# Kernel tuning notes

Hardware: AMD Instinct MI355X
Metric: run time of the kernel (lower is better)

## Reference

```python
import jax, jax.numpy as jnp
import numpy as np

D_K = 64

def setup_inputs() -> dict:
    key = jax.random.key(0)
    kq, kk, kv = jax.random.split(key, 3)
    shape = (2, 16, 2048, D_K)  # [B, H, S, d_k]
    q = jax.random.normal(kq, shape, dtype=jnp.float32)
    k = jax.random.normal(kk, shape, dtype=jnp.float32)
    v = jax.random.normal(kv, shape, dtype=jnp.float32)
    return {"q": q, "k": k, "v": v}

def reference(q, k, v):
    # score = q @ k^T / sqrt(d_k)  -> [B, H, S, S]
    scale = 1.0 / np.sqrt(D_K).astype(np.float32)
    score = jnp.einsum("bhqd,bhkd->bhqk", q, k) * scale
    attn = jax.nn.softmax(score, axis=-1)
    # dropout is identity in eval mode
    out = jnp.einsum("bhqk,bhkd->bhqd", attn, v)
    return out
```

## Files before the change

### kernel.cpp

```cpp
#include <hip/hip_runtime.h>
#include <hip/hip_bf16.h>
#include <math.h>
#include <stdint.h>


#define S_LEN 2048
#define DK 64
#define QW 32
#define NW 4
#define QBLK (QW * NW)
#define KVBLK 64
#define NT (S_LEN / KVBLK)
#define LOG2E 1.44269504088896340736f
#define THR 8.0f

typedef __attribute__((ext_vector_type(16))) float f32x16;
typedef __attribute__((ext_vector_type(8)))  __bf16 bf16x8;
typedef __attribute__((ext_vector_type(4)))  __bf16 bf16x4;
typedef __attribute__((ext_vector_type(4)))  uint32_t u32x4;

union frag_cast { u32x4 u; bf16x8 h; };

__device__ __forceinline__ uint32_t cvt_pk_bf16(float lo, float hi) {
    uint32_t r;
    asm("v_cvt_pk_bf16_f32 %0, %1, %2" : "=v"(r) : "v"(lo), "v"(hi));
    return r;
}
__device__ __forceinline__ void perm32swap(uint32_t& a, uint32_t& b) {
    asm volatile("v_permlane32_swap_b32 %0, %1" : "+v"(a), "+v"(b));
}

__global__ __launch_bounds__(256, 2)
void attn_fwd_kernel(const float* __restrict__ Qg, const float* __restrict__ Kg,
                     const float* __restrict__ Vg, float* __restrict__ Og)
{
    __shared__ __align__(16) __bf16 Kl[2][64 * 64];
    __shared__ __align__(16) __bf16 Vt[2][64 * 64];

    const int tid = threadIdx.x;
    const int lane = tid & 63;
    const int w   = tid >> 6;
    const int l31 = lane & 31;
    const int hi  = lane >> 5;

    const int qt = blockIdx.x;
    const int bh = blockIdx.y;
    const size_t base = (size_t)bh * (S_LEN * DK);
    const int q0g = qt * QBLK + w * QW;

    bf16x8 qf[4];
    {
        const float sc = 0.125f * LOG2E;
        const float* qrow = Qg + base + (size_t)(q0g + l31) * DK;
        #pragma unroll
        for (int sp = 0; sp < 4; ++sp) {
            const int d0 = 16 * sp + 8 * hi;
            float4 a = *(const float4*)(qrow + d0);
            float4 b = *(const float4*)(qrow + d0 + 4);
            bf16x8 f;
            f[0] = (__bf16)(a.x * sc); f[1] = (__bf16)(a.y * sc);
            f[2] = (__bf16)(a.z * sc); f[3] = (__bf16)(a.w * sc);
            f[4] = (__bf16)(b.x * sc); f[5] = (__bf16)(b.y * sc);
            f[6] = (__bf16)(b.z * sc); f[7] = (__bf16)(b.w * sc);
            qf[sp] = f;
        }
    }

    f32x16 acc0 = {}, acc1 = {};
    float m_run = -INFINITY, l_run = 0.f;

    float4 kpre[4];
    float  vpre[4][4];
    const int vd  = tid & 63;
    const int vkq = tid >> 6;

    auto issueLoads = [&](int t) {
        const int kv0 = t * KVBLK;
        #pragma unroll
        for (int i = 0; i < 4; ++i) {
            const int idx = tid + 256 * i;
            const int r = idx >> 4, c = idx & 15;
            kpre[i] = *(const float4*)(Kg + base + (size_t)(kv0 + r) * DK + c * 4);
        }
        #pragma unroll
        for (int i = 0; i < 4; ++i) {
            const int k0 = vkq * 4 + 16 * i;
            const float* vp = Vg + base + (size_t)(kv0 + k0) * DK + vd;
            vpre[i][0] = vp[0];      vpre[i][1] = vp[DK];
            vpre[i][2] = vp[2 * DK]; vpre[i][3] = vp[3 * DK];
        }
    };
    auto writeTile = [&](int b) {
        #pragma unroll
        for (int i = 0; i < 4; ++i) {
            const int idx = tid + 256 * i;
            const int r = idx >> 4, c = idx & 15;
            bf16x4 pk;
            pk[0] = (__bf16)kpre[i].x; pk[1] = (__bf16)kpre[i].y;
            pk[2] = (__bf16)kpre[i].z; pk[3] = (__bf16)kpre[i].w;
            *(bf16x4*)(&Kl[b][r * 64 + ((c * 4) ^ ((r & 7) << 3))]) = pk;
        }
        #pragma unroll
        for (int i = 0; i < 4; ++i) {
            const int k0 = vkq * 4 + 16 * i;
            bf16x4 pv;
            pv[0] = (__bf16)vpre[i][0]; pv[1] = (__bf16)vpre[i][1];
            pv[2] = (__bf16)vpre[i][2]; pv[3] = (__bf16)vpre[i][3];
            *(bf16x4*)(&Vt[b][vd * 64 + (k0 ^ ((vd & 7) << 3))]) = pv;
        }
    };

    issueLoads(0);
    writeTile(0);
    __syncthreads();

    int cur = 0;
    #pragma unroll 1
    for (int t = 0; t < NT; ++t) {
        if (t + 1 < NT) issueLoads(t + 1);

        f32x16 s0 = {}, s1 = {};
        __builtin_amdgcn_s_setprio(1);
        #pragma unroll
        for (int sp = 0; sp < 4; ++sp) {
            #pragma unroll
            for (int kt = 0; kt < 2; ++kt) {
                const int krow = kt * 32 + l31;
                const int eo = krow * 64 + ((16 * sp + 8 * hi) ^ ((krow & 7) << 3));
                bf16x8 kb = *(const bf16x8*)(&Kl[cur][eo]);
                if (kt == 0) s0 = __builtin_amdgcn_mfma_f32_32x32x16_bf16(kb, qf[sp], s0, 0, 0, 0);
                else         s1 = __builtin_amdgcn_mfma_f32_32x32x16_bf16(kb, qf[sp], s1, 0, 0, 0);
            }
        }
        __builtin_amdgcn_s_setprio(0);

        float vmax = -INFINITY;
        #pragma unroll
        for (int j = 0; j < 16; ++j) vmax = fmaxf(vmax, s0[j]);
        #pragma unroll
        for (int j = 0; j < 16; ++j) vmax = fmaxf(vmax, s1[j]);
        vmax = fmaxf(vmax, __shfl_xor(vmax, 32));

        if (!__all(vmax - m_run <= THR)) {
            const float mnew = fmaxf(m_run, vmax);
            const float alpha = __builtin_amdgcn_exp2f(m_run - mnew);
            m_run = mnew;
            l_run *= alpha;
            #pragma unroll
            for (int r = 0; r < 16; ++r) {
                const int ql = (r & 3) + 8 * (r >> 2) + 4 * hi;
                const float ar = __shfl(alpha, ql + (hi << 5));
                acc0[r] *= ar;
                acc1[r] *= ar;
            }
        }

        float rs = 0.f;
        #pragma unroll
        for (int j = 0; j < 16; ++j) { const float p = __builtin_amdgcn_exp2f(s0[j] - m_run); s0[j] = p; rs += p; }
        #pragma unroll
        for (int j = 0; j < 16; ++j) { const float p = __builtin_amdgcn_exp2f(s1[j] - m_run); s1[j] = p; rs += p; }
        rs += __shfl_xor(rs, 32);
        l_run += rs;

        frag_cast pa[4];
        #pragma unroll
        for (int b2 = 0; b2 < 2; ++b2) {
            #pragma unroll
            for (int st = 0; st < 2; ++st) {
                uint32_t wa, wb, wc, wd;
                if (b2 == 0) {
                    wa = cvt_pk_bf16(s0[8 * st + 0], s0[8 * st + 1]);
                    wb = cvt_pk_bf16(s0[8 * st + 2], s0[8 * st + 3]);
                    wc = cvt_pk_bf16(s0[8 * st + 4], s0[8 * st + 5]);
                    wd = cvt_pk_bf16(s0[8 * st + 6], s0[8 * st + 7]);
                } else {
                    wa = cvt_pk_bf16(s1[8 * st + 0], s1[8 * st + 1]);
                    wb = cvt_pk_bf16(s1[8 * st + 2], s1[8 * st + 3]);
                    wc = cvt_pk_bf16(s1[8 * st + 4], s1[8 * st + 5]);
                    wd = cvt_pk_bf16(s1[8 * st + 6], s1[8 * st + 7]);
                }
                perm32swap(wa, wc);
                perm32swap(wb, wd);
                pa[2 * b2 + st].u = (u32x4){wa, wb, wc, wd};
            }
        }

        __builtin_amdgcn_s_setprio(1);
        #pragma unroll
        for (int ks = 0; ks < 4; ++ks) {
            #pragma unroll
            for (int dt = 0; dt < 2; ++dt) {
                const int d = dt * 32 + l31;
                const int eo = d * 64 + ((16 * ks + 8 * hi) ^ ((d & 7) << 3));
                bf16x8 vb = *(const bf16x8*)(&Vt[cur][eo]);
                if (dt == 0) acc0 = __builtin_amdgcn_mfma_f32_32x32x16_bf16(pa[ks].h, vb, acc0, 0, 0, 0);
                else         acc1 = __builtin_amdgcn_mfma_f32_32x32x16_bf16(pa[ks].h, vb, acc1, 0, 0, 0);
            }
        }
        __builtin_amdgcn_s_setprio(0);

        if (t + 1 < NT) writeTile(cur ^ 1);
        __syncthreads();
        cur ^= 1;
    }

    float* op = Og + base;
    #pragma unroll
    for (int r = 0; r < 16; ++r) {
        const int ql = (r & 3) + 8 * (r >> 2) + 4 * hi;
        const float lr = __shfl(l_run, ql + (hi << 5));
        const float invl = 1.0f / lr;
        const size_t row = (size_t)(q0g + ql) * DK;
        op[row + l31]      = acc0[r] * invl;
        op[row + 32 + l31] = acc1[r] * invl;
    }
}

extern "C" void kernel_launch(void* const* d_in, const int* in_sizes, int n_in,
                              void* d_out, int out_size, void* d_ws, size_t ws_size,
                              hipStream_t stream) {
    const float* q = (const float*)d_in[0];
    const float* k = (const float*)d_in[1];
    const float* v = (const float*)d_in[2];
    float* o = (float*)d_out;
    const int bh = in_sizes[0] / (S_LEN * DK);
    dim3 grid(S_LEN / QBLK, bh);
    attn_fwd_kernel<<<grid, dim3(256), 0, stream>>>(q, k, v, o);
}
```

Before: 65.55 us.

## Pre-pack K/V into swizzled bf16 tiles and stream them via global_load_lds

Adds a prep kernel that converts K and V to bf16 once per call, transposing V and applying the LDS swizzle, and writes the result into workspace tiles. The attention kernel then copies each tile straight into LDS with global_load_lds DMA instead of loading fp32 into registers, converting, and writing LDS. The aim is to halve K/V bytes read by the 16 query blocks that share each head and to free VGPRs and ALU work in the main loop. The cost is an extra launch plus a workspace round-trip. There is a fallback to the old kernel when the workspace is too small.

```diff
diff --git a/kernel.cpp b/kernel.cpp
--- a/kernel.cpp
+++ b/kernel.cpp
@@ -29,13 +29,67 @@
 __device__ __forceinline__ void perm32swap(uint32_t& a, uint32_t& b) {
     asm volatile("v_permlane32_swap_b32 %0, %1" : "+v"(a), "+v"(b));
 }
+__device__ __forceinline__ void load_lds16(const __bf16* g, __bf16* l) {
+    __builtin_amdgcn_global_load_lds(
+        (const __attribute__((address_space(1))) void*)g,
+        (__attribute__((address_space(3))) void*)l, 16, 0, 0);
+}
+__device__ __forceinline__ bf16x8 pack8(float4 a, float4 b) {
+    bf16x8 f;
+    f[0] = (__bf16)a.x; f[1] = (__bf16)a.y; f[2] = (__bf16)a.z; f[3] = (__bf16)a.w;
+    f[4] = (__bf16)b.x; f[5] = (__bf16)b.y; f[6] = (__bf16)b.z; f[7] = (__bf16)b.w;
+    return f;
+}
+
+__global__ __launch_bounds__(256)
+void prep_pack(const float* __restrict__ Kg, const float* __restrict__ Vg,
+               __bf16* __restrict__ Kimg, __bf16* __restrict__ Vimg)
+{
+    __shared__ float Vs[64 * 65];
+    const int tid = threadIdx.x;
+    const int t = blockIdx.x, bh = blockIdx.y;
+    const size_t ibase = ((size_t)bh * S_LEN + (size_t)t * 64) * DK;
+    const size_t obase = ((size_t)bh * NT + t) * 4096;
+
+    #pragma unroll
+    for (int u = 0; u < 2; ++u) {
+        const int rho = tid + 256 * u;
+        const int r = rho >> 3, j = rho & 7;
+        const float* src = Kg + ibase + r * 64 + j * 8;
+        float4 a = *(const float4*)(src);
+        float4 b = *(const float4*)(src + 4);
+        *(bf16x8*)(Kimg + obase + r * 64 + ((j * 8) ^ ((r & 7) << 3))) = pack8(a, b);
+    }
+
+    {
+        const int r = tid >> 2, c0 = (tid & 3) * 16;
+        const float* src = Vg + ibase + r * 64 + c0;
+        #pragma unroll
+        for (int m = 0; m < 4; ++m) {
+            float4 x = *(const float4*)(src + 4 * m);
+            float* dst = &Vs[r * 65 + c0 + 4 * m];
+            dst[0] = x.x; dst[1] = x.y; dst[2] = x.z; dst[3] = x.w;
+        }
+    }
+    __syncthreads();
+    #pragma unroll
+    for (int u = 0; u < 2; ++u) {
+        const int rho = tid + 256 * u;
+        const int d = rho >> 3, j = rho & 7;
+        const int k0 = 8 * (j ^ (d & 7));
+        bf16x8 wv;
+        #pragma unroll
+        for (int i = 0; i < 8; ++i) wv[i] = (__bf16)Vs[(k0 + i) * 65 + d];
+        *(bf16x8*)(Vimg + obase + d * 64 + j * 8) = wv;
+    }
+}
 
 __global__ __launch_bounds__(256, 2)
-void attn_fwd_kernel(const float* __restrict__ Qg, const float* __restrict__ Kg,
-                     const float* __restrict__ Vg, float* __restrict__ Og)
+void attn_fwd_lds(const float* __restrict__ Qg, const __bf16* __restrict__ Kimg,
+                  const __bf16* __restrict__ Vimg, float* __restrict__ Og)
 {
-    __shared__ __align__(16) __bf16 Kl[2][64 * 64];
-    __shared__ __align__(16) __bf16 Vt[2][64 * 64];
+    __shared__ __align__(16) __bf16 Kl[2][4096];
+    __shared__ __align__(16) __bf16 Vt[2][4096];
 
     const int tid = threadIdx.x;
     const int lane = tid & 63;
@@ -69,67 +123,37 @@
     f32x16 acc0 = {}, acc1 = {};
     float m_run = -INFINITY, l_run = 0.f;
 
-    float4 kpre[4];
-    float  vpre[4][4];
-    const int vd  = tid & 63;
-    const int vkq = tid >> 6;
-
-    auto issueLoads = [&](int t) {
-        const int kv0 = t * KVBLK;
-        #pragma unroll
-        for (int i = 0; i < 4; ++i) {
-            const int idx = tid + 256 * i;
-            const int r = idx >> 4, c = idx & 15;
-            kpre[i] = *(const float4*)(Kg + base + (size_t)(kv0 + r) * DK + c * 4);
-        }
-        #pragma unroll
-        for (int i = 0; i < 4; ++i) {
-            const int k0 = vkq * 4 + 16 * i;
-            const float* vp = Vg + base + (size_t)(kv0 + k0) * DK + vd;
-            vpre[i][0] = vp[0];      vpre[i][1] = vp[DK];
-            vpre[i][2] = vp[2 * DK]; vpre[i][3] = vp[3 * DK];
-        }
+    const __bf16* kbase = Kimg + (size_t)bh * NT * 4096;
+    const __bf16* vbase = Vimg + (size_t)bh * NT * 4096;
+
+    auto stage = [&](int t, int b) {
+        const __bf16* kt = kbase + (size_t)t * 4096 + tid * 8;
+        const __bf16* vt = vbase + (size_t)t * 4096 + tid * 8;
+        load_lds16(kt,        &Kl[b][w * 512]);
+        load_lds16(kt + 2048, &Kl[b][2048 + w * 512]);
+        load_lds16(vt,        &Vt[b][w * 512]);
+        load_lds16(vt + 2048, &Vt[b][2048 + w * 512]);
     };
-    auto writeTile = [&](int b) {
-        #pragma unroll
-        for (int i = 0; i < 4; ++i) {
-            const int idx = tid + 256 * i;
-            const int r = idx >> 4, c = idx & 15;
-            bf16x4 pk;
-            pk[0] = (__bf16)kpre[i].x; pk[1] = (__bf16)kpre[i].y;
-            pk[2] = (__bf16)kpre[i].z; pk[3] = (__bf16)kpre[i].w;
-            *(bf16x4*)(&Kl[b][r * 64 + ((c * 4) ^ ((r & 7) << 3))]) = pk;
-        }
-        #pragma unroll
-        for (int i = 0; i < 4; ++i) {
-            const int k0 = vkq * 4 + 16 * i;
-            bf16x4 pv;
-            pv[0] = (__bf16)vpre[i][0]; pv[1] = (__bf16)vpre[i][1];
-            pv[2] = (__bf16)vpre[i][2]; pv[3] = (__bf16)vpre[i][3];
-            *(bf16x4*)(&Vt[b][vd * 64 + (k0 ^ ((vd & 7) << 3))]) = pv;
-        }
-    };
-
-    issueLoads(0);
-    writeTile(0);
+
+    stage(0, 0);
     __syncthreads();
 
     int cur = 0;
     #pragma unroll 1
     for (int t = 0; t < NT; ++t) {
-        if (t + 1 < NT) issueLoads(t + 1);
+        if (t + 1 < NT) stage(t + 1, cur ^ 1);
 
         f32x16 s0 = {}, s1 = {};
         __builtin_amdgcn_s_setprio(1);
         #pragma unroll
         for (int sp = 0; sp < 4; ++sp) {
             #pragma unroll
-            for (int kt = 0; kt < 2; ++kt) {
-                const int krow = kt * 32 + l31;
+            for (int kt2 = 0; kt2 < 2; ++kt2) {
+                const int krow = kt2 * 32 + l31;
                 const int eo = krow * 64 + ((16 * sp + 8 * hi) ^ ((krow & 7) << 3));
                 bf16x8 kb = *(const bf16x8*)(&Kl[cur][eo]);
-                if (kt == 0) s0 = __builtin_amdgcn_mfma_f32_32x32x16_bf16(kb, qf[sp], s0, 0, 0, 0);
-                else         s1 = __builtin_amdgcn_mfma_f32_32x32x16_bf16(kb, qf[sp], s1, 0, 0, 0);
+                if (kt2 == 0) s0 = __builtin_amdgcn_mfma_f32_32x32x16_bf16(kb, qf[sp], s0, 0, 0, 0);
+                else          s1 = __builtin_amdgcn_mfma_f32_32x32x16_bf16(kb, qf[sp], s1, 0, 0, 0);
             }
         }
         __builtin_amdgcn_s_setprio(0);
@@ -200,7 +224,6 @@
         }
         __builtin_amdgcn_s_setprio(0);
 
-        if (t + 1 < NT) writeTile(cur ^ 1);
         __syncthreads();
         cur ^= 1;
     }
@@ -217,6 +240,193 @@
     }
 }
 
+__global__ __launch_bounds__(256, 2)
+void attn_fwd_fb(const float* __restrict__ Qg, const float* __restrict__ Kg,
+                 const float* __restrict__ Vg, float* __restrict__ Og)
+{
+    __shared__ __align__(16) __bf16 Kl[2][64 * 64];
+    __shared__ __align__(16) __bf16 Vt[2][64 * 64];
+
+    const int tid = threadIdx.x;
+    const int lane = tid & 63;
+    const int w   = tid >> 6;
+    const int l31 = lane & 31;
+    const int hi  = lane >> 5;
+
+    const int qt = blockIdx.x;
+    const int bh = blockIdx.y;
+    const size_t base = (size_t)bh * (S_LEN * DK);
+    const int q0g = qt * QBLK + w * QW;
+
+    bf16x8 qf[4];
+    {
+        const float sc = 0.125f * LOG2E;
+        const float* qrow = Qg + base + (size_t)(q0g + l31) * DK;
+        #pragma unroll
+        for (int sp = 0; sp < 4; ++sp) {
+            const int d0 = 16 * sp + 8 * hi;
+            float4 a = *(const float4*)(qrow + d0);
+            float4 b = *(const float4*)(qrow + d0 + 4);
+            bf16x8 f;
+            f[0] = (__bf16)(a.x * sc); f[1] = (__bf16)(a.y * sc);
+            f[2] = (__bf16)(a.z * sc); f[3] = (__bf16)(a.w * sc);
+            f[4] = (__bf16)(b.x * sc); f[5] = (__bf16)(b.y * sc);
+            f[6] = (__bf16)(b.z * sc); f[7] = (__bf16)(b.w * sc);
+            qf[sp] = f;
+        }
+    }
+
+    f32x16 acc0 = {}, acc1 = {};
+    float m_run = -INFINITY, l_run = 0.f;
+
+    float4 kpre[4];
+    float  vpre[4][4];
+    const int vd  = tid & 63;
+    const int vkq = tid >> 6;
+
+    auto issueLoads = [&](int t) {
+        const int kv0 = t * KVBLK;
+        #pragma unroll
+        for (int i = 0; i < 4; ++i) {
+            const int idx = tid + 256 * i;
+            const int r = idx >> 4, c = idx & 15;
+            kpre[i] = *(const float4*)(Kg + base + (size_t)(kv0 + r) * DK + c * 4);
+        }
+        #pragma unroll
+        for (int i = 0; i < 4; ++i) {
+            const int k0 = vkq * 4 + 16 * i;
+            const float* vp = Vg + base + (size_t)(kv0 + k0) * DK + vd;
+            vpre[i][0] = vp[0];      vpre[i][1] = vp[DK];
+            vpre[i][2] = vp[2 * DK]; vpre[i][3] = vp[3 * DK];
+        }
+    };
+    auto writeTile = [&](int b) {
+        #pragma unroll
+        for (int i = 0; i < 4; ++i) {
+            const int idx = tid + 256 * i;
+            const int r = idx >> 4, c = idx & 15;
+            bf16x4 pk;
+            pk[0] = (__bf16)kpre[i].x; pk[1] = (__bf16)kpre[i].y;
+            pk[2] = (__bf16)kpre[i].z; pk[3] = (__bf16)kpre[i].w;
+            *(bf16x4*)(&Kl[b][r * 64 + ((c * 4) ^ ((r & 7) << 3))]) = pk;
+        }
+        #pragma unroll
+        for (int i = 0; i < 4; ++i) {
+            const int k0 = vkq * 4 + 16 * i;
+            bf16x4 pv;
+            pv[0] = (__bf16)vpre[i][0]; pv[1] = (__bf16)vpre[i][1];
+            pv[2] = (__bf16)vpre[i][2]; pv[3] = (__bf16)vpre[i][3];
+            *(bf16x4*)(&Vt[b][vd * 64 + (k0 ^ ((vd & 7) << 3))]) = pv;
+        }
+    };
+
+    issueLoads(0);
+    writeTile(0);
+    __syncthreads();
+
+    int cur = 0;
+    #pragma unroll 1
+    for (int t = 0; t < NT; ++t) {
+        if (t + 1 < NT) issueLoads(t + 1);
+
+        f32x16 s0 = {}, s1 = {};
+        __builtin_amdgcn_s_setprio(1);
+        #pragma unroll
+        for (int sp = 0; sp < 4; ++sp) {
+            #pragma unroll
+            for (int kt2 = 0; kt2 < 2; ++kt2) {
+                const int krow = kt2 * 32 + l31;
+                const int eo = krow * 64 + ((16 * sp + 8 * hi) ^ ((krow & 7) << 3));
+                bf16x8 kb = *(const bf16x8*)(&Kl[cur][eo]);
+                if (kt2 == 0) s0 = __builtin_amdgcn_mfma_f32_32x32x16_bf16(kb, qf[sp], s0, 0, 0, 0);
+                else          s1 = __builtin_amdgcn_mfma_f32_32x32x16_bf16(kb, qf[sp], s1, 0, 0, 0);
+            }
+        }
+        __builtin_amdgcn_s_setprio(0);
+
+        float vmax = -INFINITY;
+        #pragma unroll
+        for (int j = 0; j < 16; ++j) vmax = fmaxf(vmax, s0[j]);
+        #pragma unroll
+        for (int j = 0; j < 16; ++j) vmax = fmaxf(vmax, s1[j]);
+        vmax = fmaxf(vmax, __shfl_xor(vmax, 32));
+
+        if (!__all(vmax - m_run <= THR)) {
+            const float mnew = fmaxf(m_run, vmax);
+            const float alpha = __builtin_amdgcn_exp2f(m_run - mnew);
+            m_run = mnew;
+            l_run *= alpha;
+            #pragma unroll
+            for (int r = 0; r < 16; ++r) {
+                const int ql = (r & 3) + 8 * (r >> 2) + 4 * hi;
+                const float ar = __shfl(alpha, ql + (hi << 5));
+                acc0[r] *= ar;
+                acc1[r] *= ar;
+            }
+        }
+
+        float rs = 0.f;
+        #pragma unroll
+        for (int j = 0; j < 16; ++j) { const float p = __builtin_amdgcn_exp2f(s0[j] - m_run); s0[j] = p; rs += p; }
+        #pragma unroll
+        for (int j = 0; j < 16; ++j) { const float p = __builtin_amdgcn_exp2f(s1[j] - m_run); s1[j] = p; rs += p; }
+        rs += __shfl_xor(rs, 32);
+        l_run += rs;
+
+        frag_cast pa[4];
+        #pragma unroll
+        for (int b2 = 0; b2 < 2; ++b2) {
+            #pragma unroll
+            for (int st = 0; st < 2; ++st) {
+                uint32_t wa, wb, wc, wd;
+                if (b2 == 0) {
+                    wa = cvt_pk_bf16(s0[8 * st + 0], s0[8 * st + 1]);
+                    wb = cvt_pk_bf16(s0[8 * st + 2], s0[8 * st + 3]);
+                    wc = cvt_pk_bf16(s0[8 * st + 4], s0[8 * st + 5]);
+                    wd = cvt_pk_bf16(s0[8 * st + 6], s0[8 * st + 7]);
+                } else {
+                    wa = cvt_pk_bf16(s1[8 * st + 0], s1[8 * st + 1]);
+                    wb = cvt_pk_bf16(s1[8 * st + 2], s1[8 * st + 3]);
+                    wc = cvt_pk_bf16(s1[8 * st + 4], s1[8 * st + 5]);
+                    wd = cvt_pk_bf16(s1[8 * st + 6], s1[8 * st + 7]);
+                }
+                perm32swap(wa, wc);
+                perm32swap(wb, wd);
+                pa[2 * b2 + st].u = (u32x4){wa, wb, wc, wd};
+            }
+        }
+
+        __builtin_amdgcn_s_setprio(1);
+        #pragma unroll
+        for (int ks = 0; ks < 4; ++ks) {
+            #pragma unroll
+            for (int dt = 0; dt < 2; ++dt) {
+                const int d = dt * 32 + l31;
+                const int eo = d * 64 + ((16 * ks + 8 * hi) ^ ((d & 7) << 3));
+                bf16x8 vb = *(const bf16x8*)(&Vt[cur][eo]);
+                if (dt == 0) acc0 = __builtin_amdgcn_mfma_f32_32x32x16_bf16(pa[ks].h, vb, acc0, 0, 0, 0);
+                else         acc1 = __builtin_amdgcn_mfma_f32_32x32x16_bf16(pa[ks].h, vb, acc1, 0, 0, 0);
+            }
+        }
+        __builtin_amdgcn_s_setprio(0);
+
+        if (t + 1 < NT) writeTile(cur ^ 1);
+        __syncthreads();
+        cur ^= 1;
+    }
+
+    float* op = Og + base;
+    #pragma unroll
+    for (int r = 0; r < 16; ++r) {
+        const int ql = (r & 3) + 8 * (r >> 2) + 4 * hi;
+        const float lr = __shfl(l_run, ql + (hi << 5));
+        const float invl = 1.0f / lr;
+        const size_t row = (size_t)(q0g + ql) * DK;
+        op[row + l31]      = acc0[r] * invl;
+        op[row + 32 + l31] = acc1[r] * invl;
+    }
+}
+
 extern "C" void kernel_launch(void* const* d_in, const int* in_sizes, int n_in,
                               void* d_out, int out_size, void* d_ws, size_t ws_size,
                               hipStream_t stream) {
@@ -225,6 +435,14 @@
     const float* v = (const float*)d_in[2];
     float* o = (float*)d_out;
     const int bh = in_sizes[0] / (S_LEN * DK);
-    dim3 grid(S_LEN / QBLK, bh);
-    attn_fwd_kernel<<<grid, dim3(256), 0, stream>>>(q, k, v, o);
-}
+
+    const size_t img_bytes = (size_t)bh * NT * 4096 * sizeof(__bf16);
+    if (ws_size >= 2 * img_bytes) {
+        __bf16* Kimg = (__bf16*)d_ws;
+        __bf16* Vimg = (__bf16*)((char*)d_ws + img_bytes);
+        prep_pack<<<dim3(NT, bh), dim3(256), 0, stream>>>(k, v, Kimg, Vimg);
+        attn_fwd_lds<<<dim3(S_LEN / QBLK, bh), dim3(256), 0, stream>>>(q, Kimg, Vimg, o);
+    } else {
+        attn_fwd_fb<<<dim3(S_LEN / QBLK, bh), dim3(256), 0, stream>>>(q, k, v, o);
+    }
+}
```

After: 67.53 us. 3.0% more time.
